# Performance work log

Measured on AMD Instinct MI355X. Metric: run time of the kernel, lower is better.

Reference implementation:

```python
import jax, jax.numpy as jnp
import numpy as np

NUM_CAPS = 10
DIM_CAPS = 16
ROUTINGS = 3


def setup_inputs() -> dict:
    key = jax.random.key(0)
    k1, k2 = jax.random.split(key)
    x = jax.random.normal(k1, (128, 1152, 512), dtype=jnp.float32)
    # glorot-uniform-ish scale for W [D_in, num_caps*dim_caps]
    limit = (6.0 / (512 + NUM_CAPS * DIM_CAPS)) ** 0.5
    W = jax.random.uniform(k2, (512, NUM_CAPS * DIM_CAPS), dtype=jnp.float32,
                           minval=-limit, maxval=limit)
    return {"x": x, "W": W}


def _squash(s, axis=-1):
    # s_norm = ||s|| + 1e-7; out = s_norm^2/(1+s_norm^2) * s/s_norm
    s_norm = jnp.linalg.norm(s, axis=axis, keepdims=True) + 1e-7
    return (s_norm ** 2) / (1.0 + s_norm ** 2) * (s / s_norm)


def reference(x, W):
    B, N, _ = x.shape
    # u_hat: [B, N, C, D]
    u_hat = jnp.matmul(x, W).reshape(B, N, NUM_CAPS, DIM_CAPS)
    b = jnp.zeros((B, N, NUM_CAPS), dtype=u_hat.dtype)
    v = None
    for i in range(ROUTINGS):
        c = jax.nn.softmax(b, axis=2)                      # [B, N, C]
        s = jnp.einsum('bnc,bncd->bcd', c, u_hat)          # [B, C, D]
        v = _squash(s)                                     # [B, C, D]
        if i < ROUTINGS - 1:
            b = b + jnp.einsum('bncd,bcd->bnc', u_hat, v)
    return v
```

## Files before the change

kernel.cpp:

```cpp
#include <hip/hip_runtime.h>

#define BB 128
#define NN 1152
#define KD 512
#define NC 10
#define ND 16
#define CD 160

typedef unsigned short ushort_t;
typedef unsigned int uint_t;
typedef short short8v __attribute__((ext_vector_type(8)));
typedef float float4v __attribute__((ext_vector_type(4)));
typedef float float16v __attribute__((ext_vector_type(16)));

__device__ __forceinline__ float bf2f(ushort_t u) {
  return __uint_as_float(((uint_t)u) << 16);
}
__device__ __forceinline__ ushort_t f2bf(float f) {
  uint_t x = __float_as_uint(f);
  x += 0x7fffu + ((x >> 16) & 1u);
  return (ushort_t)(x >> 16);
}

#define BAR_LDS() do {                                   \
    __builtin_amdgcn_sched_barrier(0);                   \
    asm volatile("s_waitcnt lgkmcnt(0)" ::: "memory");   \
    __builtin_amdgcn_s_barrier();                        \
    __builtin_amdgcn_sched_barrier(0);                   \
  } while (0)

__global__ __launch_bounds__(256) void wconv(const float* __restrict__ W,
                                             ushort_t* __restrict__ Wt) {
  int idx = blockIdx.x * 256 + threadIdx.x;
  int n = idx >> 9, k = idx & 511;
  Wt[idx] = f2bf(W[(size_t)k * CD + n]);
}

__global__ __launch_bounds__(256, 2) void gemm_mfma(
    const float* __restrict__ x, const ushort_t* __restrict__ Wt,
    ushort_t* __restrict__ uhat, float* __restrict__ partials) {
  __shared__ __align__(16) char smem[73728];
  const int tid = threadIdx.x;
  const int wid = tid >> 6, lane = tid & 63;
  const int l31 = lane & 31, lh = lane >> 5;
  const int row0 = blockIdx.x * 128;

  float16v acc[5];
#pragma unroll
  for (int nt = 0; nt < 5; ++nt)
#pragma unroll
    for (int r = 0; r < 16; ++r) acc[nt][r] = 0.f;

  int aby[4];
#pragma unroll
  for (int i = 0; i < 4; ++i) {
    int f = tid + i * 256;
    int ar = f >> 3, s = f & 7;
    aby[i] = (ar << 7) + ((s ^ (ar & 7)) << 4);
  }
  const int arow_ = tid >> 3;
  const int akq = tid & 7;
  int bsrc[5], bby[5];
#pragma unroll
  for (int i = 0; i < 5; ++i) {
    int f = tid + i * 256;
    int br = f >> 3, bs = f & 7;
    bsrc[i] = br * KD + bs * 8;
    bby[i] = (br << 7) + ((bs ^ (br & 7)) << 4);
  }

  float4v rA[4][2];
  short8v rB[5];

  auto LOADS = [&](int ks) {
    int k0 = ks * 64;
#pragma unroll
    for (int i = 0; i < 4; ++i) {
      const float* p = x + (size_t)(row0 + arow_ + i * 32) * KD + k0 + akq * 8;
      rA[i][0] = *reinterpret_cast<const float4v*>(p);
      rA[i][1] = *reinterpret_cast<const float4v*>(p + 4);
    }
#pragma unroll
    for (int i = 0; i < 5; ++i)
      rB[i] = *reinterpret_cast<const short8v*>(Wt + bsrc[i] + k0);
  };
  auto WRITES = [&](int buf) {
    char* Ab = smem + buf * 16384;
    char* Bb = smem + 32768 + buf * 20480;
#pragma unroll
    for (int i = 0; i < 4; ++i) {
      short8v pk;
#pragma unroll
      for (int e = 0; e < 4; ++e) {
        pk[e] = (short)f2bf(rA[i][0][e]);
        pk[e + 4] = (short)f2bf(rA[i][1][e]);
      }
      *reinterpret_cast<short8v*>(Ab + aby[i]) = pk;
    }
#pragma unroll
    for (int i = 0; i < 5; ++i)
      *reinterpret_cast<short8v*>(Bb + bby[i]) = rB[i];
  };

  const int arow = wid * 32 + l31;
  const int arx = (arow & 7);
  LOADS(0);
  WRITES(0);
  LOADS(1);
  BAR_LDS();
  int cur = 0;
  for (int ks = 0; ks < 8; ++ks) {
    const char* Ab = smem + cur * 16384;
    const char* Bb = smem + 32768 + cur * 20480;
#pragma unroll
    for (int ss = 0; ss < 4; ++ss) {
      int slot = ss * 2 + lh;
      short8v a = *reinterpret_cast<const short8v*>(
          Ab + (arow << 7) + ((slot ^ arx) << 4));
#pragma unroll
      for (int nt = 0; nt < 5; ++nt) {
        int brow = nt * 32 + l31;
        short8v bfr = *reinterpret_cast<const short8v*>(
            Bb + (brow << 7) + ((slot ^ (brow & 7)) << 4));
        acc[nt] = __builtin_amdgcn_mfma_f32_32x32x16_bf16(a, bfr, acc[nt], 0, 0, 0);
      }
    }
    if (ks < 7) {
      WRITES(cur ^ 1);
      if (ks < 6) LOADS(ks + 2);
    }
    BAR_LDS();
    cur ^= 1;
  }

  float* sAf = reinterpret_cast<float*>(smem + 43008);
#pragma unroll
  for (int nt = 0; nt < 5; ++nt) {
    float p = 0.f;
#pragma unroll
    for (int r = 0; r < 16; ++r) p += acc[nt][r];
    p += __shfl_xor(p, 32);
    if (lh == 0) sAf[wid * CD + nt * 32 + l31] = p;
  }

  ushort_t* Ct = reinterpret_cast<ushort_t*>(smem);
#pragma unroll
  for (int nt = 0; nt < 5; ++nt)
#pragma unroll
    for (int r = 0; r < 16; ++r) {
      int row = wid * 32 + (r & 3) + 8 * (r >> 2) + 4 * lh;
      Ct[row * 168 + nt * 32 + l31] = f2bf(acc[nt][r]);
    }
  __syncthreads();
  if (tid < CD) {
    float s = sAf[tid] + sAf[CD + tid] + sAf[2 * CD + tid] + sAf[3 * CD + tid];
    partials[(size_t)blockIdx.x * CD + tid] = s;
  }
#pragma unroll
  for (int i = 0; i < 10; ++i) {
    int p = tid + i * 256;
    int row = p / 20, c0 = (p % 20) * 8;
    *reinterpret_cast<short8v*>(&uhat[(size_t)(row0 + row) * CD + c0]) =
        *reinterpret_cast<const short8v*>(&Ct[row * 168 + c0]);
  }
}

#define ITER_T 640
template <int ITER2>
__global__ __launch_bounds__(ITER_T) void iter_k(
    const ushort_t* __restrict__ uhat, const float* __restrict__ pg,
    const float* __restrict__ p1, float* __restrict__ pout) {
  __shared__ float bv[128][NC];
  __shared__ float wv[128][NC];
  __shared__ float sred[32][CD];
  __shared__ float sred2[4][CD];
  __shared__ float vv[CD];
  const int blk = blockIdx.x;
  const int b = blk / 9, ch = blk % 9;
  const int t = threadIdx.x;
  const int g = t / 20, q = t % 20;
  const int c = q >> 1;
  const ushort_t* ub = uhat + ((size_t)b * NN + ch * 128) * CD + q * 8;

  if (t < CD) {
    float s0 = 0.f;
#pragma unroll
    for (int cc = 0; cc < 9; ++cc) s0 += pg[((size_t)b * 9 + cc) * CD + t];
    s0 *= 0.1f;
    float ss = s0 * s0;
    ss += __shfl_xor(ss, 1); ss += __shfl_xor(ss, 2);
    ss += __shfl_xor(ss, 4); ss += __shfl_xor(ss, 8);
    float sn = sqrtf(ss) + 1e-7f;
    float v = s0 * sn / (1.f + sn * sn);
    if (ITER2) {
      float s1 = 0.f;
#pragma unroll
      for (int cc = 0; cc < 9; ++cc) s1 += p1[((size_t)b * 9 + cc) * CD + t];
      float ss1 = s1 * s1;
      ss1 += __shfl_xor(ss1, 1); ss1 += __shfl_xor(ss1, 2);
      ss1 += __shfl_xor(ss1, 4); ss1 += __shfl_xor(ss1, 8);
      float sn1 = sqrtf(ss1) + 1e-7f;
      v += s1 * sn1 / (1.f + sn1 * sn1);
    }
    vv[t] = v;
  }
  __syncthreads();

  float v0r[8];
  {
    float4v a = *reinterpret_cast<const float4v*>(&vv[q * 8]);
    float4v bb = *reinterpret_cast<const float4v*>(&vv[q * 8 + 4]);
#pragma unroll
    for (int e = 0; e < 4; ++e) { v0r[e] = a[e]; v0r[e + 4] = bb[e]; }
  }

  short8v u8[4];
#pragma unroll
  for (int it = 0; it < 4; ++it) {
    int n = g + it * 32;
    u8[it] = *reinterpret_cast<const short8v*>(ub + (size_t)n * CD);
    float p = 0.f;
#pragma unroll
    for (int e = 0; e < 8; ++e) p += bf2f((ushort_t)u8[it][e]) * v0r[e];
    p += __shfl_xor(p, 1);
    if ((q & 1) == 0) bv[n][c] = p;
  }
  __syncthreads();

  if (t < 128) {
    float e[NC];
    float bm = bv[t][0];
#pragma unroll
    for (int cc = 1; cc < NC; ++cc) bm = fmaxf(bm, bv[t][cc]);
    float Z = 0.f;
#pragma unroll
    for (int cc = 0; cc < NC; ++cc) { e[cc] = __expf(bv[t][cc] - bm); Z += e[cc]; }
    float rz = 1.f / Z;
#pragma unroll
    for (int cc = 0; cc < NC; ++cc) wv[t][cc] = e[cc] * rz;
  }
  __syncthreads();

  float a[8];
#pragma unroll
  for (int e = 0; e < 8; ++e) a[e] = 0.f;
#pragma unroll
  for (int it = 0; it < 4; ++it) {
    int n = g + it * 32;
    float w = wv[n][c];
#pragma unroll
    for (int e = 0; e < 8; ++e) a[e] += w * bf2f((ushort_t)u8[it][e]);
  }
  {
    float4v lo, hi;
#pragma unroll
    for (int e = 0; e < 4; ++e) { lo[e] = a[e]; hi[e] = a[e + 4]; }
    float4v* dst = reinterpret_cast<float4v*>(&sred[g][q * 8]);
    dst[0] = lo; dst[1] = hi;
  }
  __syncthreads();
  {
    int col = t % CD, part = t / CD;
    float s = 0.f;
#pragma unroll
    for (int g8 = 0; g8 < 8; ++g8) s += sred[part * 8 + g8][col];
    sred2[part][col] = s;
  }
  __syncthreads();
  if (t < CD) {
    pout[(size_t)blk * CD + t] =
        sred2[0][t] + sred2[1][t] + sred2[2][t] + sred2[3][t];
  }
}

__global__ __launch_bounds__(CD) void squash_out(
    const float* __restrict__ p2, float* __restrict__ outp) {
  int b = blockIdx.x, t = threadIdx.x;
  float s = 0.f;
#pragma unroll
  for (int cc = 0; cc < 9; ++cc) s += p2[((size_t)b * 9 + cc) * CD + t];
  float ss = s * s;
  ss += __shfl_xor(ss, 1); ss += __shfl_xor(ss, 2);
  ss += __shfl_xor(ss, 4); ss += __shfl_xor(ss, 8);
  float sn = sqrtf(ss) + 1e-7f;
  outp[(size_t)b * CD + t] = s * sn / (1.f + sn * sn);
}

extern "C" void kernel_launch(void* const* d_in, const int* in_sizes, int n_in,
                              void* d_out, int out_size, void* d_ws, size_t ws_size,
                              hipStream_t stream) {
  const float* x = (const float*)d_in[0];
  const float* W = (const float*)d_in[1];
  float* out = (float*)d_out;

  char* ws = (char*)d_ws;
  ushort_t* uhat = (ushort_t*)ws;
  ushort_t* Wt   = (ushort_t*)(ws + 47185920);
  float*    pg   = (float*)(ws + 47349760);
  float*    p1   = (float*)(ws + 48087040);
  float*    p2   = (float*)(ws + 48824320);

  wconv<<<320, 256, 0, stream>>>(W, Wt);
  gemm_mfma<<<1152, 256, 0, stream>>>(x, Wt, uhat, pg);
  iter_k<0><<<1152, ITER_T, 0, stream>>>(uhat, pg, nullptr, p1);
  iter_k<1><<<1152, ITER_T, 0, stream>>>(uhat, pg, p1, p2);
  squash_out<<<BB, CD, 0, stream>>>(p2, out);
}
```

Before: 103.1 us.

## Halve GEMM K-tile and LDS footprint to raise occupancy to four blocks

Shrinks the GEMM K-step from 64 to 32 so the double-buffered A/B LDS tiles drop from 72KB to 36KB, and raises launch bounds to allow four blocks per CU. The swizzle is adapted to 64-byte rows, and the bf16 output staging is split into two 64-row halves so it fits in the smaller LDS. This aims to hide global load latency through more concurrent blocks, at the cost of twice as many loop iterations and barriers and a tighter register budget per thread.

```diff
diff --git a/kernel.cpp b/kernel.cpp
--- a/kernel.cpp
+++ b/kernel.cpp
@@ -36,10 +36,10 @@
   Wt[idx] = f2bf(W[(size_t)k * CD + n]);
 }
 
-__global__ __launch_bounds__(256, 2) void gemm_mfma(
+__global__ __launch_bounds__(256, 4) void gemm_mfma(
     const float* __restrict__ x, const ushort_t* __restrict__ Wt,
     ushort_t* __restrict__ uhat, float* __restrict__ partials) {
-  __shared__ __align__(16) char smem[73728];
+  __shared__ __align__(16) char smem[36864];
   const int tid = threadIdx.x;
   const int wid = tid >> 6, lane = tid & 63;
   const int l31 = lane & 31, lh = lane >> 5;
@@ -51,44 +51,44 @@
 #pragma unroll
     for (int r = 0; r < 16; ++r) acc[nt][r] = 0.f;
 
-  int aby[4];
-#pragma unroll
-  for (int i = 0; i < 4; ++i) {
+  int aby[2], arsrc[2];
+#pragma unroll
+  for (int i = 0; i < 2; ++i) {
+    int u = tid + i * 256;
+    int ar = u >> 2, hs = u & 3;
+    arsrc[i] = ar * KD + hs * 8;
+    aby[i] = (ar << 6) + ((hs ^ ((ar >> 1) & 3)) << 4);
+  }
+  int bsrc[3], bby[3];
+#pragma unroll
+  for (int i = 0; i < 3; ++i) {
     int f = tid + i * 256;
-    int ar = f >> 3, s = f & 7;
-    aby[i] = (ar << 7) + ((s ^ (ar & 7)) << 4);
-  }
-  const int arow_ = tid >> 3;
-  const int akq = tid & 7;
-  int bsrc[5], bby[5];
-#pragma unroll
-  for (int i = 0; i < 5; ++i) {
-    int f = tid + i * 256;
-    int br = f >> 3, bs = f & 7;
+    int br = (f >> 2) % 160, bs = f & 3;
     bsrc[i] = br * KD + bs * 8;
-    bby[i] = (br << 7) + ((bs ^ (br & 7)) << 4);
-  }
-
-  float4v rA[4][2];
-  short8v rB[5];
+    bby[i] = (br << 6) + ((bs ^ ((br >> 1) & 3)) << 4);
+  }
+  const bool b2ok = tid < 128;
+
+  float4v rA[2][2];
+  short8v rB[3];
 
   auto LOADS = [&](int ks) {
-    int k0 = ks * 64;
-#pragma unroll
-    for (int i = 0; i < 4; ++i) {
-      const float* p = x + (size_t)(row0 + arow_ + i * 32) * KD + k0 + akq * 8;
+    int k0 = ks * 32;
+#pragma unroll
+    for (int i = 0; i < 2; ++i) {
+      const float* p = x + (size_t)row0 * KD + arsrc[i] + k0;
       rA[i][0] = *reinterpret_cast<const float4v*>(p);
       rA[i][1] = *reinterpret_cast<const float4v*>(p + 4);
     }
-#pragma unroll
-    for (int i = 0; i < 5; ++i)
-      rB[i] = *reinterpret_cast<const short8v*>(Wt + bsrc[i] + k0);
+    rB[0] = *reinterpret_cast<const short8v*>(Wt + bsrc[0] + k0);
+    rB[1] = *reinterpret_cast<const short8v*>(Wt + bsrc[1] + k0);
+    if (b2ok) rB[2] = *reinterpret_cast<const short8v*>(Wt + bsrc[2] + k0);
   };
   auto WRITES = [&](int buf) {
-    char* Ab = smem + buf * 16384;
-    char* Bb = smem + 32768 + buf * 20480;
-#pragma unroll
-    for (int i = 0; i < 4; ++i) {
+    char* Ab = smem + buf * 8192;
+    char* Bb = smem + 16384 + buf * 10240;
+#pragma unroll
+    for (int i = 0; i < 2; ++i) {
       short8v pk;
 #pragma unroll
       for (int e = 0; e < 4; ++e) {
@@ -97,43 +97,43 @@
       }
       *reinterpret_cast<short8v*>(Ab + aby[i]) = pk;
     }
-#pragma unroll
-    for (int i = 0; i < 5; ++i)
-      *reinterpret_cast<short8v*>(Bb + bby[i]) = rB[i];
+    *reinterpret_cast<short8v*>(Bb + bby[0]) = rB[0];
+    *reinterpret_cast<short8v*>(Bb + bby[1]) = rB[1];
+    if (b2ok) *reinterpret_cast<short8v*>(Bb + bby[2]) = rB[2];
   };
 
   const int arow = wid * 32 + l31;
-  const int arx = (arow & 7);
+  const int arx = (arow >> 1) & 3;
   LOADS(0);
   WRITES(0);
   LOADS(1);
   BAR_LDS();
   int cur = 0;
-  for (int ks = 0; ks < 8; ++ks) {
-    const char* Ab = smem + cur * 16384;
-    const char* Bb = smem + 32768 + cur * 20480;
-#pragma unroll
-    for (int ss = 0; ss < 4; ++ss) {
+  for (int ks = 0; ks < 16; ++ks) {
+    const char* Ab = smem + cur * 8192;
+    const char* Bb = smem + 16384 + cur * 10240;
+#pragma unroll
+    for (int ss = 0; ss < 2; ++ss) {
       int slot = ss * 2 + lh;
       short8v a = *reinterpret_cast<const short8v*>(
-          Ab + (arow << 7) + ((slot ^ arx) << 4));
+          Ab + (arow << 6) + ((slot ^ arx) << 4));
 #pragma unroll
       for (int nt = 0; nt < 5; ++nt) {
         int brow = nt * 32 + l31;
         short8v bfr = *reinterpret_cast<const short8v*>(
-            Bb + (brow << 7) + ((slot ^ (brow & 7)) << 4));
+            Bb + (brow << 6) + ((slot ^ ((brow >> 1) & 3)) << 4));
         acc[nt] = __builtin_amdgcn_mfma_f32_32x32x16_bf16(a, bfr, acc[nt], 0, 0, 0);
       }
     }
-    if (ks < 7) {
+    if (ks < 15) {
       WRITES(cur ^ 1);
-      if (ks < 6) LOADS(ks + 2);
+      if (ks < 14) LOADS(ks + 2);
     }
     BAR_LDS();
     cur ^= 1;
   }
 
-  float* sAf = reinterpret_cast<float*>(smem + 43008);
+  float* sAf = reinterpret_cast<float*>(smem + 32768);
 #pragma unroll
   for (int nt = 0; nt < 5; ++nt) {
     float p = 0.f;
@@ -142,26 +142,35 @@
     p += __shfl_xor(p, 32);
     if (lh == 0) sAf[wid * CD + nt * 32 + l31] = p;
   }
-
-  ushort_t* Ct = reinterpret_cast<ushort_t*>(smem);
-#pragma unroll
-  for (int nt = 0; nt < 5; ++nt)
-#pragma unroll
-    for (int r = 0; r < 16; ++r) {
-      int row = wid * 32 + (r & 3) + 8 * (r >> 2) + 4 * lh;
-      Ct[row * 168 + nt * 32 + l31] = f2bf(acc[nt][r]);
-    }
   __syncthreads();
   if (tid < CD) {
     float s = sAf[tid] + sAf[CD + tid] + sAf[2 * CD + tid] + sAf[3 * CD + tid];
     partials[(size_t)blockIdx.x * CD + tid] = s;
   }
-#pragma unroll
-  for (int i = 0; i < 10; ++i) {
-    int p = tid + i * 256;
-    int row = p / 20, c0 = (p % 20) * 8;
-    *reinterpret_cast<short8v*>(&uhat[(size_t)(row0 + row) * CD + c0]) =
-        *reinterpret_cast<const short8v*>(&Ct[row * 168 + c0]);
+
+  ushort_t* Ct = reinterpret_cast<ushort_t*>(smem);
+#pragma unroll
+  for (int h = 0; h < 2; ++h) {
+    if ((wid >> 1) == h) {
+      int rbase = (wid & 1) * 32;
+#pragma unroll
+      for (int nt = 0; nt < 5; ++nt)
+#pragma unroll
+        for (int r = 0; r < 16; ++r) {
+          int row = rbase + (r & 3) + 8 * (r >> 2) + 4 * lh;
+          Ct[row * 168 + nt * 32 + l31] = f2bf(acc[nt][r]);
+        }
+    }
+    __syncthreads();
+#pragma unroll
+    for (int i = 0; i < 5; ++i) {
+      int p = tid + i * 256;
+      int row = p / 20, c0 = (p % 20) * 8;
+      *reinterpret_cast<short8v*>(
+          &uhat[(size_t)(row0 + h * 64 + row) * CD + c0]) =
+          *reinterpret_cast<const short8v*>(&Ct[row * 168 + c0]);
+    }
+    if (h == 0) __syncthreads();
   }
 }
 
```

New measurement: 181.0 us. 1.76x slower.

## Load A operand directly from global into MFMA registers, skipping LDS staging

Applied to the files above, without the earlier changes.

Removes the LDS staging of the fp32 input tile: each lane now loads its own row segment of x directly, converts to bf16 in registers, and feeds the MFMA, with a one-step register prefetch. Only the W tile remains double-buffered in shared memory, shrinking the LDS footprint. This cuts LDS writes/reads and barrier pressure for A, but global reads of x become per-lane strided rows with shorter prefetch distance, which may hurt coalescing and latency hiding.

```diff
diff --git a/kernel.cpp b/kernel.cpp
--- a/kernel.cpp
+++ b/kernel.cpp
@@ -39,7 +39,7 @@
 __global__ __launch_bounds__(256, 2) void gemm_mfma(
     const float* __restrict__ x, const ushort_t* __restrict__ Wt,
     ushort_t* __restrict__ uhat, float* __restrict__ partials) {
-  __shared__ __align__(16) char smem[73728];
+  __shared__ __align__(16) char smem[45568];
   const int tid = threadIdx.x;
   const int wid = tid >> 6, lane = tid & 63;
   const int l31 = lane & 31, lh = lane >> 5;
@@ -51,15 +51,6 @@
 #pragma unroll
     for (int r = 0; r < 16; ++r) acc[nt][r] = 0.f;
 
-  int aby[4];
-#pragma unroll
-  for (int i = 0; i < 4; ++i) {
-    int f = tid + i * 256;
-    int ar = f >> 3, s = f & 7;
-    aby[i] = (ar << 7) + ((s ^ (ar & 7)) << 4);
-  }
-  const int arow_ = tid >> 3;
-  const int akq = tid & 7;
   int bsrc[5], bby[5];
 #pragma unroll
   for (int i = 0; i < 5; ++i) {
@@ -68,66 +59,58 @@
     bsrc[i] = br * KD + bs * 8;
     bby[i] = (br << 7) + ((bs ^ (br & 7)) << 4);
   }
-
-  float4v rA[4][2];
   short8v rB[5];
 
-  auto LOADS = [&](int ks) {
+  auto LOADSB = [&](int ks) {
     int k0 = ks * 64;
-#pragma unroll
-    for (int i = 0; i < 4; ++i) {
-      const float* p = x + (size_t)(row0 + arow_ + i * 32) * KD + k0 + akq * 8;
-      rA[i][0] = *reinterpret_cast<const float4v*>(p);
-      rA[i][1] = *reinterpret_cast<const float4v*>(p + 4);
-    }
 #pragma unroll
     for (int i = 0; i < 5; ++i)
       rB[i] = *reinterpret_cast<const short8v*>(Wt + bsrc[i] + k0);
   };
-  auto WRITES = [&](int buf) {
-    char* Ab = smem + buf * 16384;
-    char* Bb = smem + 32768 + buf * 20480;
-#pragma unroll
-    for (int i = 0; i < 4; ++i) {
-      short8v pk;
-#pragma unroll
-      for (int e = 0; e < 4; ++e) {
-        pk[e] = (short)f2bf(rA[i][0][e]);
-        pk[e + 4] = (short)f2bf(rA[i][1][e]);
-      }
-      *reinterpret_cast<short8v*>(Ab + aby[i]) = pk;
-    }
+  auto WRITESB = [&](int buf) {
+    char* Bb = smem + buf * 20480;
 #pragma unroll
     for (int i = 0; i < 5; ++i)
       *reinterpret_cast<short8v*>(Bb + bby[i]) = rB[i];
   };
 
-  const int arow = wid * 32 + l31;
-  const int arx = (arow & 7);
-  LOADS(0);
-  WRITES(0);
-  LOADS(1);
+  const float* abase = x + (size_t)(row0 + wid * 32 + l31) * KD + lh * 8;
+
+  LOADSB(0);
+  WRITESB(0);
+  LOADSB(1);
+  float4v fa0 = *reinterpret_cast<const float4v*>(abase);
+  float4v fa1 = *reinterpret_cast<const float4v*>(abase + 4);
   BAR_LDS();
   int cur = 0;
   for (int ks = 0; ks < 8; ++ks) {
-    const char* Ab = smem + cur * 16384;
-    const char* Bb = smem + 32768 + cur * 20480;
+    const char* Bb = smem + cur * 20480;
 #pragma unroll
     for (int ss = 0; ss < 4; ++ss) {
+      int nks = ks, nss = ss + 1;
+      if (nss == 4) { nss = 0; nks = (ks < 7) ? ks + 1 : 7; }
+      const float* np = abase + nks * 64 + nss * 16;
+      float4v nb0 = *reinterpret_cast<const float4v*>(np);
+      float4v nb1 = *reinterpret_cast<const float4v*>(np + 4);
+      short8v af;
+#pragma unroll
+      for (int e = 0; e < 4; ++e) {
+        af[e] = (short)f2bf(fa0[e]);
+        af[e + 4] = (short)f2bf(fa1[e]);
+      }
       int slot = ss * 2 + lh;
-      short8v a = *reinterpret_cast<const short8v*>(
-          Ab + (arow << 7) + ((slot ^ arx) << 4));
 #pragma unroll
       for (int nt = 0; nt < 5; ++nt) {
         int brow = nt * 32 + l31;
         short8v bfr = *reinterpret_cast<const short8v*>(
             Bb + (brow << 7) + ((slot ^ (brow & 7)) << 4));
-        acc[nt] = __builtin_amdgcn_mfma_f32_32x32x16_bf16(a, bfr, acc[nt], 0, 0, 0);
+        acc[nt] = __builtin_amdgcn_mfma_f32_32x32x16_bf16(af, bfr, acc[nt], 0, 0, 0);
       }
+      fa0 = nb0; fa1 = nb1;
     }
     if (ks < 7) {
-      WRITES(cur ^ 1);
-      if (ks < 6) LOADS(ks + 2);
+      WRITESB(cur ^ 1);
+      if (ks < 6) LOADSB(ks + 2);
     }
     BAR_LDS();
     cur ^= 1;
```

New measurement: 123.8 us. 20.1% more time.

## Load W tile directly into LDS via global_load_lds and pack bf16 pairs

Applied to the files above, without the earlier changes.

Replaces the register-staged W tile loads and LDS stores with direct global-to-LDS loads (global_load_lds, 16 bytes each), issued one k-step ahead with explicit vmcnt waits. The float-to-bf16 conversion of x now uses the packed two-value intrinsic instead of manual per-element rounding. The sAf scratch region moves beyond the double-buffered area, which makes LDS slightly larger. The goal is to cut VGPR pressure and VALU/LDS-store instructions in the GEMM main loop. The hand-counted vmcnt thresholds could be fragile.

```diff
diff --git a/kernel.cpp b/kernel.cpp
--- a/kernel.cpp
+++ b/kernel.cpp
@@ -1,4 +1,5 @@
 #include <hip/hip_runtime.h>
+#include <hip/hip_bf16.h>
 
 #define BB 128
 #define NN 1152
@@ -12,22 +13,26 @@
 typedef short short8v __attribute__((ext_vector_type(8)));
 typedef float float4v __attribute__((ext_vector_type(4)));
 typedef float float16v __attribute__((ext_vector_type(16)));
+typedef uint_t uint4v __attribute__((ext_vector_type(4)));
 
 __device__ __forceinline__ float bf2f(ushort_t u) {
   return __uint_as_float(((uint_t)u) << 16);
 }
 __device__ __forceinline__ ushort_t f2bf(float f) {
-  uint_t x = __float_as_uint(f);
-  x += 0x7fffu + ((x >> 16) & 1u);
-  return (ushort_t)(x >> 16);
-}
-
-#define BAR_LDS() do {                                   \
-    __builtin_amdgcn_sched_barrier(0);                   \
-    asm volatile("s_waitcnt lgkmcnt(0)" ::: "memory");   \
-    __builtin_amdgcn_s_barrier();                        \
-    __builtin_amdgcn_sched_barrier(0);                   \
-  } while (0)
+  __hip_bfloat16 h = __float2bfloat16(f);
+  union { __hip_bfloat16 h; ushort_t u; } cv; cv.h = h; return cv.u;
+}
+__device__ __forceinline__ uint_t pk2(float a, float b) {
+  float2 f; f.x = a; f.y = b;
+  __hip_bfloat162 h = __float22bfloat162_rn(f);
+  union { __hip_bfloat162 h; uint_t u; } cv; cv.h = h; return cv.u;
+}
+
+#define SBAR() __builtin_amdgcn_sched_barrier(0)
+#define GLOAD_LDS16(gp, lp)                                        \
+  __builtin_amdgcn_global_load_lds(                                \
+      (const __attribute__((address_space(1))) void*)(gp),         \
+      (__attribute__((address_space(3))) void*)(lp), 16, 0, 0)
 
 __global__ __launch_bounds__(256) void wconv(const float* __restrict__ W,
                                              ushort_t* __restrict__ Wt) {
@@ -39,7 +44,7 @@
 __global__ __launch_bounds__(256, 2) void gemm_mfma(
     const float* __restrict__ x, const ushort_t* __restrict__ Wt,
     ushort_t* __restrict__ uhat, float* __restrict__ partials) {
-  __shared__ __align__(16) char smem[73728];
+  __shared__ __align__(16) char smem[76288];
   const int tid = threadIdx.x;
   const int wid = tid >> 6, lane = tid & 63;
   const int l31 = lane & 31, lh = lane >> 5;
@@ -60,19 +65,13 @@
   }
   const int arow_ = tid >> 3;
   const int akq = tid & 7;
-  int bsrc[5], bby[5];
-#pragma unroll
-  for (int i = 0; i < 5; ++i) {
-    int f = tid + i * 256;
-    int br = f >> 3, bs = f & 7;
-    bsrc[i] = br * KD + bs * 8;
-    bby[i] = (br << 7) + ((bs ^ (br & 7)) << 4);
-  }
+
+  const int brow_g = wid * 40 + (lane >> 3);
+  const int bslot_g = lane & 7;
 
   float4v rA[4][2];
-  short8v rB[5];
-
-  auto LOADS = [&](int ks) {
+
+  auto LOADSA = [&](int ks) {
     int k0 = ks * 64;
 #pragma unroll
     for (int i = 0; i < 4; ++i) {
@@ -80,36 +79,46 @@
       rA[i][0] = *reinterpret_cast<const float4v*>(p);
       rA[i][1] = *reinterpret_cast<const float4v*>(p + 4);
     }
-#pragma unroll
-    for (int i = 0; i < 5; ++i)
-      rB[i] = *reinterpret_cast<const short8v*>(Wt + bsrc[i] + k0);
   };
-  auto WRITES = [&](int buf) {
+  auto WRITESA = [&](int buf) {
     char* Ab = smem + buf * 16384;
-    char* Bb = smem + 32768 + buf * 20480;
 #pragma unroll
     for (int i = 0; i < 4; ++i) {
-      short8v pk;
-#pragma unroll
-      for (int e = 0; e < 4; ++e) {
-        pk[e] = (short)f2bf(rA[i][0][e]);
-        pk[e + 4] = (short)f2bf(rA[i][1][e]);
-      }
-      *reinterpret_cast<short8v*>(Ab + aby[i]) = pk;
-    }
-#pragma unroll
-    for (int i = 0; i < 5; ++i)
-      *reinterpret_cast<short8v*>(Bb + bby[i]) = rB[i];
+      uint4v p;
+      p[0] = pk2(rA[i][0][0], rA[i][0][1]);
+      p[1] = pk2(rA[i][0][2], rA[i][0][3]);
+      p[2] = pk2(rA[i][1][0], rA[i][1][1]);
+      p[3] = pk2(rA[i][1][2], rA[i][1][3]);
+      *reinterpret_cast<uint4v*>(Ab + aby[i]) = p;
+    }
   };
+  auto GLOADB = [&](int ks, int buf) {
+    int k0 = ks * 64;
+    char* lbase = smem + 32768 + buf * 20480 + wid * 5120;
+#pragma unroll
+    for (int j = 0; j < 5; ++j) {
+      int row = brow_g + j * 8;
+      int sslot = bslot_g ^ (row & 7);
+      const ushort_t* gp = Wt + row * KD + k0 + sslot * 8;
+      GLOAD_LDS16(gp, lbase + j * 1024);
+    }
+  };
 
   const int arow = wid * 32 + l31;
-  const int arx = (arow & 7);
-  LOADS(0);
-  WRITES(0);
-  LOADS(1);
-  BAR_LDS();
+  const int arx = arow & 7;
+
+  LOADSA(0);
+  WRITESA(0);
+  GLOADB(0, 0);
+  LOADSA(1);
+  SBAR();
+  asm volatile("s_waitcnt vmcnt(8) lgkmcnt(0)" ::: "memory");
+  __builtin_amdgcn_s_barrier();
+  SBAR();
+
   int cur = 0;
   for (int ks = 0; ks < 8; ++ks) {
+    if (ks < 7) GLOADB(ks + 1, cur ^ 1);
     const char* Ab = smem + cur * 16384;
     const char* Bb = smem + 32768 + cur * 20480;
 #pragma unroll
@@ -125,15 +134,21 @@
         acc[nt] = __builtin_amdgcn_mfma_f32_32x32x16_bf16(a, bfr, acc[nt], 0, 0, 0);
       }
     }
-    if (ks < 7) {
-      WRITES(cur ^ 1);
-      if (ks < 6) LOADS(ks + 2);
-    }
-    BAR_LDS();
+    if (ks < 7) WRITESA(cur ^ 1);
+    if (ks < 6) LOADSA(ks + 2);
+    SBAR();
+    if (ks < 6)
+      asm volatile("s_waitcnt vmcnt(8) lgkmcnt(0)" ::: "memory");
+    else if (ks == 6)
+      asm volatile("s_waitcnt vmcnt(0) lgkmcnt(0)" ::: "memory");
+    else
+      asm volatile("s_waitcnt lgkmcnt(0)" ::: "memory");
+    __builtin_amdgcn_s_barrier();
+    SBAR();
     cur ^= 1;
   }
 
-  float* sAf = reinterpret_cast<float*>(smem + 43008);
+  float* sAf = reinterpret_cast<float*>(smem + 73728);
 #pragma unroll
   for (int nt = 0; nt < 5; ++nt) {
     float p = 0.f;
```

After: 105.8 us. +2.7%, slower.
